# Kernel optimization log

Hardware: AMD Instinct MI355X
Metric: run time of the kernel (lower is better)

Reference implementation:

```python
import jax, jax.numpy as jnp
import numpy as np

B, S, D, U, L, DEG = 32, 256, 256, 256, 16, 16
N = B * S
E = N * DEG


def _xavier(k, shape, fan_in, fan_out):
    return jax.random.normal(k, shape, jnp.float32) * np.float32(np.sqrt(2.0 / (fan_in + fan_out)))


def setup_inputs() -> dict:
    key = jax.random.key(0)
    ks = jax.random.split(key, 16)
    src = jax.random.normal(ks[0], (S, B, D), jnp.float32)
    V_in = _xavier(ks[1], (L, D, U), D, U)
    b_in = jnp.zeros((L, U), jnp.float32)
    V_in_gate = _xavier(ks[2], (D, 1), D, 1)
    b_in_gate = jnp.ones((L, 1), jnp.float32)
    V_out = _xavier(ks[3], (L, D, U), D, U)
    b_out = jnp.zeros((L, U), jnp.float32)
    V_out_gate = _xavier(ks[4], (D, 1), D, 1)
    b_out_gate = jnp.ones((L, 1), jnp.float32)
    W_self_loop = _xavier(ks[5], (D, U), D, U)
    W_self_loop_gate = _xavier(ks[6], (D, 1), D, 1)
    arc_tensor_in = jnp.stack([jax.random.randint(ks[7], (E,), 0, B),
                               jax.random.randint(ks[8], (E,), 0, S)]).astype(jnp.int64)
    arc_tensor_out = jnp.stack([jax.random.randint(ks[9], (E,), 0, B),
                                jax.random.randint(ks[10], (E,), 0, S)]).astype(jnp.int64)
    label_tensor_in = jax.random.randint(ks[11], (1, E), 0, L).astype(jnp.int64)
    label_tensor_out = jax.random.randint(ks[12], (1, E), 0, L).astype(jnp.int64)
    mask_in = jnp.ones((N, DEG), jnp.float32)
    mask_out = jnp.ones((N, DEG), jnp.float32)
    mask_loop = jnp.ones((N, 1), jnp.float32)
    sent_mask = jnp.ones((S, B), jnp.float32)
    return {"src": src, "V_in": V_in, "b_in": b_in, "V_in_gate": V_in_gate,
            "b_in_gate": b_in_gate, "V_out": V_out, "b_out": b_out,
            "V_out_gate": V_out_gate, "b_out_gate": b_out_gate,
            "W_self_loop": W_self_loop, "W_self_loop_gate": W_self_loop_gate,
            "arc_tensor_in": arc_tensor_in, "arc_tensor_out": arc_tensor_out,
            "label_tensor_in": label_tensor_in, "label_tensor_out": label_tensor_out,
            "mask_in": mask_in, "mask_out": mask_out, "mask_loop": mask_loop,
            "sent_mask": sent_mask}


def _gcn_forward(src, V_in, b_in, V_in_gate, b_in_gate, V_out, b_out, V_out_gate,
                 b_out_gate, W_self_loop, W_self_loop_gate, mask_in, mask_out,
                 mask_loop, sent_mask, arc_tensor_in, arc_tensor_out,
                 label_tensor_in, label_tensor_out):
    S_, B_, D_ = src.shape
    U_ = V_in.shape[-1]
    enc = jnp.transpose(src, (1, 0, 2))            # [B,S,D]
    x = enc.reshape(B_ * S_, D_)                   # [N,D]

    def arc_branch(V, b, Vg, bg, arc, lab):
        # per-label transform of all nodes, as in the original: [L,N,U]
        all_lab = jnp.einsum('nd,ldu->lnu', x, V)
        idx = arc[0] * S_ + arc[1]                 # [E] flat node indices
        l = lab[0]                                  # [E] edge labels
        feats = all_lab[l, idx] + b[l]              # [E,U]
        deg = idx.shape[0] // (B_ * S_)
        feats = feats.reshape(B_, S_, deg, U_)
        g = (x @ Vg)[idx, 0] + bg[l, 0]             # [E]
        gate = g.reshape(B_, S_, deg)
        return feats, gate

    in_, in_gate = arc_branch(V_in, b_in, V_in_gate, b_in_gate, arc_tensor_in, label_tensor_in)
    out_, out_gate = arc_branch(V_out, b_out, V_out_gate, b_out_gate, arc_tensor_out, label_tensor_out)
    same = (x @ W_self_loop).reshape(B_, S_, 1, U_)
    same_gate = (x @ W_self_loop_gate).reshape(B_, S_, 1)

    pot = jnp.concatenate([in_, out_, same], axis=2)            # [B,S,maxdeg,U]
    pot_gate = jnp.concatenate([in_gate, out_gate, same_gate], axis=2)
    mask_soft = jnp.concatenate([mask_in, mask_out, mask_loop], axis=1)  # [N,maxdeg]
    md = pot.shape[2]
    pot = pot.reshape(B_ * S_, md, U_)
    probs = jax.nn.sigmoid(pot_gate.reshape(B_ * S_, md)) * mask_soft
    res = jax.nn.relu(jnp.sum(pot * probs[:, :, None], axis=1)).reshape(B_, S_, U_)
    res = res * sent_mask.T[:, :, None]
    return jnp.transpose(res, (1, 0, 2))            # [S,B,U]


def reference(src, V_in, b_in, V_in_gate, b_in_gate, V_out, b_out, V_out_gate,
              b_out_gate, W_self_loop, W_self_loop_gate, arc_tensor_in,
              arc_tensor_out, label_tensor_in, label_tensor_out, mask_in,
              mask_out, mask_loop, sent_mask):
    return _gcn_forward(src, V_in, b_in, V_in_gate, b_in_gate, V_out, b_out,
                        V_out_gate, b_out_gate, W_self_loop, W_self_loop_gate,
                        mask_in, mask_out, mask_loop, sent_mask,
                        arc_tensor_in, arc_tensor_out, label_tensor_in,
                        label_tensor_out)
```

## Files before the change

### kernel.cpp

```cpp
#include <hip/hip_runtime.h>
#include <hip/hip_bf16.h>

#define BB 32
#define SS 256
#define DD 256
#define UU 256
#define LL 16
#define DEG 16
#define NN (BB * SS)
#define EE (NN * DEG)
#define NSLICE 33
#define KMAIN (NSLICE * DD)
#define KEXT 256
#define KTOT (KMAIN + KEXT)
#define KSPLIT 8
#define KS (KTOT / KSPLIT)
#define TM 128
#define TN 256

using short8 = __attribute__((ext_vector_type(8))) short;
using f32x4  = __attribute__((ext_vector_type(4))) float;

#define GLDS(g, l)                                                        \
  __builtin_amdgcn_global_load_lds(                                       \
      (const __attribute__((address_space(1))) void*)(g),                 \
      (__attribute__((address_space(3))) void*)(l), 16, 0, 0)

__device__ __forceinline__ float bf2f(unsigned short v) {
  union { unsigned u; float f; } t;
  t.u = ((unsigned)v) << 16;
  return t.f;
}
__device__ __forceinline__ unsigned short f2bf(float f) {
  __hip_bfloat16 h = __float2bfloat16(f);
  return *(unsigned short*)&h;
}
__device__ __forceinline__ float sigm(float x) {
  return 1.f / (1.f + __expf(-x));
}

__global__ __launch_bounds__(256) void k_pre(
    const float* __restrict__ src, const float* __restrict__ gin,
    const float* __restrict__ gout, const float* __restrict__ gloop,
    const float* __restrict__ Vin, const float* __restrict__ Vout,
    const float* __restrict__ Wself, const float* __restrict__ b_in,
    const float* __restrict__ b_out,
    __hip_bfloat16* __restrict__ x_bf, float* __restrict__ xg_in,
    float* __restrict__ xg_out, float* __restrict__ xg_loop,
    __hip_bfloat16* __restrict__ Vt) {
  int bid = blockIdx.x;
  if (bid < NN) {
    int n = bid;
    int b = n / SS, s = n % SS;
    int d = threadIdx.x;
    float v = src[(size_t)(s * BB + b) * DD + d];
    x_bf[(size_t)n * DD + d] = __float2bfloat16(v);
    float p0 = v * gin[d], p1 = v * gout[d], p2 = v * gloop[d];
#pragma unroll
    for (int o = 32; o > 0; o >>= 1) {
      p0 += __shfl_down(p0, o);
      p1 += __shfl_down(p1, o);
      p2 += __shfl_down(p2, o);
    }
    __shared__ float r0[4], r1[4], r2[4];
    int w = threadIdx.x >> 6, lane = threadIdx.x & 63;
    if (lane == 0) { r0[w] = p0; r1[w] = p1; r2[w] = p2; }
    __syncthreads();
    if (threadIdx.x == 0) {
      xg_in[n]   = r0[0] + r0[1] + r0[2] + r0[3];
      xg_out[n]  = r1[0] + r1[1] + r1[2] + r1[3];
      xg_loop[n] = r2[0] + r2[1] + r2[2] + r2[3];
    }
    return;
  }
  int t = bid - NN;
  int z = t >> 6;
  int rem = t & 63;
  int bx = rem & 7, by = rem >> 3;
  int tid = threadIdx.x;
  int tx = tid & 31, ty = tid >> 5;
  if (z == NSLICE) {
    int u0 = bx * 32, j0 = by * 32;
#pragma unroll
    for (int i = 0; i < 4; i++) {
      int u = u0 + ty + i * 8, j = j0 + tx;
      float v = 0.f;
      if (j >= 1 && j <= LL)         v = b_in[(j - 1) * UU + u];
      else if (j > LL && j < NSLICE) v = b_out[(j - 1 - LL) * UU + u];
      Vt[(size_t)u * KTOT + KMAIN + j] = __float2bfloat16(v);
    }
    return;
  }
  __shared__ float tbuf[32][33];
  const float* srcM = (z == 0) ? Wself
                    : (z <= LL ? Vin  + (size_t)(z - 1)      * DD * UU
                               : Vout + (size_t)(z - 1 - LL) * DD * UU);
  int u0 = bx * 32, d0 = by * 32;
#pragma unroll
  for (int i = 0; i < 4; i++) {
    int dr = ty + i * 8;
    tbuf[dr][tx] = srcM[(size_t)(d0 + dr) * UU + u0 + tx];
  }
  __syncthreads();
#pragma unroll
  for (int i = 0; i < 4; i++) {
    int ur = ty + i * 8;
    Vt[(size_t)(u0 + ur) * KTOT + z * DD + d0 + tx] = __float2bfloat16(tbuf[tx][ur]);
  }
}

__global__ __launch_bounds__(64) void k_agg(
    const __hip_bfloat16* __restrict__ x,
    const float* __restrict__ xg_in, const float* __restrict__ xg_out,
    const float* __restrict__ xg_loop,
    const float* __restrict__ b_ing, const float* __restrict__ b_outg,
    const int* __restrict__ arc_in, const int* __restrict__ arc_out,
    const int* __restrict__ lab_in, const int* __restrict__ lab_out,
    const float* __restrict__ mask_in, const float* __restrict__ mask_out,
    const float* __restrict__ mask_loop,
    __hip_bfloat16* __restrict__ Y) {
  __shared__ int u_sl[32], u_src[32];
  __shared__ float u_w[32];
  __shared__ int s_sl[32], s_src[32];
  __shared__ float s_w[32];
  __shared__ float s_wsum[NSLICE];
  int n = blockIdx.x, tid = threadIdx.x;
  if (tid < 32) {
    int br = tid >> 4, k = tid & 15;
    int e = n * DEG + k;
    const int* a = br ? arc_out : arc_in;
    int l = (br ? lab_out : lab_in)[e];
    int srcn = a[e] * SS + a[EE + e];
    float g = (br ? xg_out : xg_in)[srcn] + (br ? b_outg : b_ing)[l];
    u_sl[tid] = 1 + br * LL + l;
    u_src[tid] = srcn;
    u_w[tid] = sigm(g) * (br ? mask_out : mask_in)[e];
  }
  __syncthreads();
  if (tid < 32) {
    int my = u_sl[tid];
    int rank = 0;
#pragma unroll
    for (int j = 0; j < 32; j++) {
      int oj = u_sl[j];
      rank += (oj < my || (oj == my && j < tid)) ? 1 : 0;
    }
    s_sl[rank] = my;
    s_src[rank] = u_src[tid];
    s_w[rank] = u_w[tid];
  }
  __syncthreads();

  const unsigned short* xp = (const unsigned short*)x;
  unsigned short* yp = (unsigned short*)Y;
  size_t base = (size_t)n * KTOT;
  int d4 = tid * 4;
  {
    float wl = sigm(xg_loop[n]) * mask_loop[n];
    ushort4 v = *(const ushort4*)&xp[(size_t)n * DD + d4];
    ushort4 o;
    o.x = f2bf(wl * bf2f(v.x)); o.y = f2bf(wl * bf2f(v.y));
    o.z = f2bf(wl * bf2f(v.z)); o.w = f2bf(wl * bf2f(v.w));
    *(ushort4*)&yp[base + d4] = o;
  }
  unsigned long long present = 0ull;
  float a0 = 0.f, a1 = 0.f, a2 = 0.f, a3 = 0.f, ws = 0.f;
#pragma unroll
  for (int e = 0; e < 32; e++) {
    int sl = s_sl[e];
    int srcn = s_src[e];
    float w = s_w[e];
    ushort4 v = *(const ushort4*)&xp[(size_t)srcn * DD + d4];
    a0 += w * bf2f(v.x); a1 += w * bf2f(v.y);
    a2 += w * bf2f(v.z); a3 += w * bf2f(v.w);
    ws += w;
    int slnext = (e < 31) ? s_sl[e + 1] : 999;
    if (sl != slnext) {
      ushort4 o;
      o.x = f2bf(a0); o.y = f2bf(a1); o.z = f2bf(a2); o.w = f2bf(a3);
      *(ushort4*)&yp[base + sl * DD + d4] = o;
      if (tid == 0) s_wsum[sl] = ws;
      present |= (1ull << sl);
      a0 = a1 = a2 = a3 = ws = 0.f;
    }
  }
  ushort4 zero4 = {0, 0, 0, 0};
#pragma unroll
  for (int s = 1; s < NSLICE; s++) {
    if (!((present >> s) & 1ull)) {
      *(ushort4*)&yp[base + s * DD + d4] = zero4;
      if (tid == 0) s_wsum[s] = 0.f;
    }
  }
  __syncthreads();
  {
    ushort4 o;
    unsigned short* op = (unsigned short*)&o;
#pragma unroll
    for (int c = 0; c < 4; c++) {
      int j = d4 + c;
      float v = (j >= 1 && j < NSLICE) ? s_wsum[j] : 0.f;
      op[c] = f2bf(v);
    }
    *(ushort4*)&yp[base + KMAIN + d4] = o;
  }
}

__global__ __launch_bounds__(256, 2) void k_gemm(
    const __hip_bfloat16* __restrict__ A, const __hip_bfloat16* __restrict__ Bt,
    __hip_bfloat16* __restrict__ partial) {
  __shared__ __align__(16) __hip_bfloat16 As[2][TM * 32];
  __shared__ __align__(16) __hip_bfloat16 Bs[2][TN * 32];
  __hip_bfloat16* P = partial + (size_t)blockIdx.y * NN * UU;
  int kbeg = blockIdx.y * KS;
  int row0 = blockIdx.x * TM;
  int tid = threadIdx.x;
  int w = tid >> 6, lane = tid & 63;
  int lrow = lane & 15, quad = lane >> 4;
  int sr = lane >> 2;
  int sc = (lane & 3) * 8;

#define STAGE(bufi, k0)                                                     \
  {                                                                         \
    _Pragma("unroll")                                                       \
    for (int t = 0; t < 2; t++) {                                           \
      int rb = (w * 2 + t) * 16;                                            \
      GLDS(&A[(size_t)(row0 + rb + sr) * KTOT + (k0) + sc],                 \
           &As[bufi][rb * 32]);                                             \
    }                                                                       \
    _Pragma("unroll")                                                       \
    for (int t = 0; t < 4; t++) {                                           \
      int rb = (w * 4 + t) * 16;                                            \
      GLDS(&Bt[(size_t)(rb + sr) * KTOT + (k0) + sc], &Bs[bufi][rb * 32]);  \
    }                                                                       \
  }

  STAGE(0, kbeg);
  f32x4 acc[8][4] = {};
  constexpr int NIT = KS / 32;
  for (int it = 0; it < NIT; it++) {
    int cur = it & 1;
    __syncthreads();
    if (it + 1 < NIT) STAGE(cur ^ 1, kbeg + (it + 1) * 32);
    short8 af[8], bfr[4];
#pragma unroll
    for (int i = 0; i < 8; i++)
      af[i] = *(const short8*)&As[cur][(i * 16 + lrow) * 32 + quad * 8];
#pragma unroll
    for (int j = 0; j < 4; j++)
      bfr[j] = *(const short8*)&Bs[cur][(w * 64 + j * 16 + lrow) * 32 + quad * 8];
#pragma unroll
    for (int j = 0; j < 4; j++)
#pragma unroll
      for (int i = 0; i < 8; i++)
        acc[i][j] = __builtin_amdgcn_mfma_f32_16x16x32_bf16(af[i], bfr[j], acc[i][j], 0, 0, 0);
  }
#undef STAGE
#pragma unroll
  for (int i = 0; i < 8; i++)
#pragma unroll
    for (int j = 0; j < 4; j++) {
      int col = w * 64 + j * 16 + lrow;
      int rowb = row0 + i * 16 + quad * 4;
#pragma unroll
      for (int r = 0; r < 4; r++)
        P[(size_t)(rowb + r) * UU + col] = __float2bfloat16(acc[i][j][r]);
    }
}

__global__ __launch_bounds__(64) void k_finish(
    const __hip_bfloat16* __restrict__ partial, const float* __restrict__ sent,
    float* __restrict__ out) {
  int n = blockIdx.x, u4 = threadIdx.x * 4;
  size_t idx = (size_t)n * UU + u4;
  const unsigned short* pp = (const unsigned short*)partial;
  float a0 = 0.f, a1 = 0.f, a2 = 0.f, a3 = 0.f;
#pragma unroll
  for (int z = 0; z < KSPLIT; z++) {
    ushort4 v = *(const ushort4*)&pp[(size_t)z * NN * UU + idx];
    a0 += bf2f(v.x); a1 += bf2f(v.y); a2 += bf2f(v.z); a3 += bf2f(v.w);
  }
  int s = n % SS, b = n / SS;
  float sm = sent[s * BB + b];
  float4 o;
  o.x = fmaxf(a0, 0.f) * sm; o.y = fmaxf(a1, 0.f) * sm;
  o.z = fmaxf(a2, 0.f) * sm; o.w = fmaxf(a3, 0.f) * sm;
  *(float4*)&out[((size_t)s * BB + b) * UU + u4] = o;
}

extern "C" void kernel_launch(void* const* d_in, const int* in_sizes, int n_in,
                              void* d_out, int out_size, void* d_ws, size_t ws_size,
                              hipStream_t stream) {
  const float* src      = (const float*)d_in[0];
  const float* V_in     = (const float*)d_in[1];
  const float* b_in     = (const float*)d_in[2];
  const float* V_ing    = (const float*)d_in[3];
  const float* b_ing    = (const float*)d_in[4];
  const float* V_out    = (const float*)d_in[5];
  const float* b_out    = (const float*)d_in[6];
  const float* V_outg   = (const float*)d_in[7];
  const float* b_outg   = (const float*)d_in[8];
  const float* W_self   = (const float*)d_in[9];
  const float* W_selfg  = (const float*)d_in[10];
  const int* arc_in     = (const int*)d_in[11];
  const int* arc_out    = (const int*)d_in[12];
  const int* lab_in     = (const int*)d_in[13];
  const int* lab_out    = (const int*)d_in[14];
  const float* mask_in  = (const float*)d_in[15];
  const float* mask_out = (const float*)d_in[16];
  const float* mask_loop= (const float*)d_in[17];
  const float* sent     = (const float*)d_in[18];
  float* out = (float*)d_out;

  char* ws = (char*)d_ws;
  size_t off = 0;
  auto alloc = [&](size_t bytes) -> void* {
    void* p = ws + off;
    off += (bytes + 255) & ~(size_t)255;
    return p;
  };
  __hip_bfloat16* x_bf = (__hip_bfloat16*)alloc((size_t)NN * DD * 2);
  __hip_bfloat16* Vt   = (__hip_bfloat16*)alloc((size_t)UU * KTOT * 2);
  float* xg_in   = (float*)alloc(NN * 4);
  float* xg_out  = (float*)alloc(NN * 4);
  float* xg_loop = (float*)alloc(NN * 4);
  __hip_bfloat16* Y = (__hip_bfloat16*)alloc((size_t)NN * KTOT * 2);
  __hip_bfloat16* partial =
      (__hip_bfloat16*)alloc((size_t)KSPLIT * NN * UU * 2);

  k_pre<<<NN + (NSLICE + 1) * 64, 256, 0, stream>>>(
      src, V_ing, V_outg, W_selfg, V_in, V_out, W_self, b_in, b_out,
      x_bf, xg_in, xg_out, xg_loop, Vt);
  k_agg<<<NN, 64, 0, stream>>>(x_bf, xg_in, xg_out, xg_loop, b_ing, b_outg,
                               arc_in, arc_out, lab_in, lab_out,
                               mask_in, mask_out, mask_loop, Y);
  k_gemm<<<dim3(NN / TM, KSPLIT), 256, 0, stream>>>(Y, Vt, partial);
  k_finish<<<NN, 64, 0, stream>>>(partial, sent, out);
}
```

Measured before the change: 192.4 us.

## Fuse neighbor aggregation into GEMM A-tile construction, drop materialized Y

Instead of materializing the large aggregated matrix Y (N x ~8.7K bf16) in a separate kernel, a small metadata kernel writes sorted edge lists, per-slice offsets and weight sums. The GEMM then builds each A tile on the fly by gathering source rows of x and weighting them, with K split into 17 chunks of two slices each and the M tile reduced to 64 rows. This removes the write and re-read of Y, but adds irregular gathers inside the GEMM main loop and a larger partial buffer for k_finish to reduce.

```diff
diff --git a/kernel.cpp b/kernel.cpp
--- a/kernel.cpp
+++ b/kernel.cpp
@@ -13,9 +13,8 @@
 #define KMAIN (NSLICE * DD)
 #define KEXT 256
 #define KTOT (KMAIN + KEXT)
-#define KSPLIT 8
-#define KS (KTOT / KSPLIT)
-#define TM 128
+#define KSPLIT 17
+#define TM 64
 #define TN 256
 
 using short8 = __attribute__((ext_vector_type(8))) short;
@@ -109,8 +108,7 @@
   }
 }
 
-__global__ __launch_bounds__(64) void k_agg(
-    const __hip_bfloat16* __restrict__ x,
+__global__ __launch_bounds__(64) void k_meta(
     const float* __restrict__ xg_in, const float* __restrict__ xg_out,
     const float* __restrict__ xg_loop,
     const float* __restrict__ b_ing, const float* __restrict__ b_outg,
@@ -118,12 +116,10 @@
     const int* __restrict__ lab_in, const int* __restrict__ lab_out,
     const float* __restrict__ mask_in, const float* __restrict__ mask_out,
     const float* __restrict__ mask_loop,
-    __hip_bfloat16* __restrict__ Y) {
+    int2* __restrict__ ed, unsigned char* __restrict__ off,
+    float* __restrict__ wsumbuf) {
   __shared__ int u_sl[32], u_src[32];
   __shared__ float u_w[32];
-  __shared__ int s_sl[32], s_src[32];
-  __shared__ float s_w[32];
-  __shared__ float s_wsum[NSLICE];
   int n = blockIdx.x, tid = threadIdx.x;
   if (tid < 32) {
     int br = tid >> 4, k = tid & 15;
@@ -145,106 +141,97 @@
       int oj = u_sl[j];
       rank += (oj < my || (oj == my && j < tid)) ? 1 : 0;
     }
-    s_sl[rank] = my;
-    s_src[rank] = u_src[tid];
-    s_w[rank] = u_w[tid];
-  }
-  __syncthreads();
-
-  const unsigned short* xp = (const unsigned short*)x;
-  unsigned short* yp = (unsigned short*)Y;
-  size_t base = (size_t)n * KTOT;
-  int d4 = tid * 4;
-  {
+    ed[(size_t)n * 34 + 1 + rank] =
+        make_int2(u_src[tid] | (my << 16), __float_as_int(u_w[tid]));
+  }
+  if (tid == 32) {
     float wl = sigm(xg_loop[n]) * mask_loop[n];
-    ushort4 v = *(const ushort4*)&xp[(size_t)n * DD + d4];
-    ushort4 o;
-    o.x = f2bf(wl * bf2f(v.x)); o.y = f2bf(wl * bf2f(v.y));
-    o.z = f2bf(wl * bf2f(v.z)); o.w = f2bf(wl * bf2f(v.w));
-    *(ushort4*)&yp[base + d4] = o;
-  }
-  unsigned long long present = 0ull;
-  float a0 = 0.f, a1 = 0.f, a2 = 0.f, a3 = 0.f, ws = 0.f;
-#pragma unroll
-  for (int e = 0; e < 32; e++) {
-    int sl = s_sl[e];
-    int srcn = s_src[e];
-    float w = s_w[e];
-    ushort4 v = *(const ushort4*)&xp[(size_t)srcn * DD + d4];
-    a0 += w * bf2f(v.x); a1 += w * bf2f(v.y);
-    a2 += w * bf2f(v.z); a3 += w * bf2f(v.w);
-    ws += w;
-    int slnext = (e < 31) ? s_sl[e + 1] : 999;
-    if (sl != slnext) {
-      ushort4 o;
-      o.x = f2bf(a0); o.y = f2bf(a1); o.z = f2bf(a2); o.w = f2bf(a3);
-      *(ushort4*)&yp[base + sl * DD + d4] = o;
-      if (tid == 0) s_wsum[sl] = ws;
-      present |= (1ull << sl);
-      a0 = a1 = a2 = a3 = ws = 0.f;
-    }
-  }
-  ushort4 zero4 = {0, 0, 0, 0};
-#pragma unroll
-  for (int s = 1; s < NSLICE; s++) {
-    if (!((present >> s) & 1ull)) {
-      *(ushort4*)&yp[base + s * DD + d4] = zero4;
-      if (tid == 0) s_wsum[s] = 0.f;
-    }
-  }
-  __syncthreads();
-  {
-    ushort4 o;
-    unsigned short* op = (unsigned short*)&o;
-#pragma unroll
-    for (int c = 0; c < 4; c++) {
-      int j = d4 + c;
-      float v = (j >= 1 && j < NSLICE) ? s_wsum[j] : 0.f;
-      op[c] = f2bf(v);
-    }
-    *(ushort4*)&yp[base + KMAIN + d4] = o;
-  }
-}
-
-__global__ __launch_bounds__(256, 2) void k_gemm(
-    const __hip_bfloat16* __restrict__ A, const __hip_bfloat16* __restrict__ Bt,
-    __hip_bfloat16* __restrict__ partial) {
+    ed[(size_t)n * 34] = make_int2(n, __float_as_int(wl));
+  }
+  if (tid < 35) {
+    int cnt = 0;
+#pragma unroll
+    for (int j = 0; j < 32; j++) cnt += (u_sl[j] < tid) ? 1 : 0;
+    off[(size_t)n * 36 + tid] = (unsigned char)((tid >= 1 ? 1 : 0) + cnt);
+  }
+  float ws = 0.f;
+  if (tid >= 1 && tid < 33) {
+#pragma unroll
+    for (int j = 0; j < 32; j++) ws += (u_sl[j] == tid) ? u_w[j] : 0.f;
+  }
+  if (tid < 34) wsumbuf[(size_t)n * 34 + tid] = ws;
+}
+
+__global__ __launch_bounds__(256, 3) void k_gemm(
+    const __hip_bfloat16* __restrict__ x, const __hip_bfloat16* __restrict__ Bt,
+    const int2* __restrict__ ed, const unsigned char* __restrict__ off,
+    const float* __restrict__ wsumbuf, __hip_bfloat16* __restrict__ partial) {
   __shared__ __align__(16) __hip_bfloat16 As[2][TM * 32];
   __shared__ __align__(16) __hip_bfloat16 Bs[2][TN * 32];
-  __hip_bfloat16* P = partial + (size_t)blockIdx.y * NN * UU;
-  int kbeg = blockIdx.y * KS;
+  int z = blockIdx.y;
+  __hip_bfloat16* P = partial + (size_t)z * NN * UU;
   int row0 = blockIdx.x * TM;
   int tid = threadIdx.x;
   int w = tid >> 6, lane = tid & 63;
   int lrow = lane & 15, quad = lane >> 4;
-  int sr = lane >> 2;
-  int sc = (lane & 3) * 8;
-
-#define STAGE(bufi, k0)                                                     \
-  {                                                                         \
-    _Pragma("unroll")                                                       \
-    for (int t = 0; t < 2; t++) {                                           \
-      int rb = (w * 2 + t) * 16;                                            \
-      GLDS(&A[(size_t)(row0 + rb + sr) * KTOT + (k0) + sc],                 \
-           &As[bufi][rb * 32]);                                             \
-    }                                                                       \
-    _Pragma("unroll")                                                       \
-    for (int t = 0; t < 4; t++) {                                           \
-      int rb = (w * 4 + t) * 16;                                            \
-      GLDS(&Bt[(size_t)(rb + sr) * KTOT + (k0) + sc], &Bs[bufi][rb * 32]);  \
-    }                                                                       \
-  }
-
-  STAGE(0, kbeg);
-  f32x4 acc[8][4] = {};
-  constexpr int NIT = KS / 32;
+  int sr = lane >> 2, sc = (lane & 3) * 8;
+  int r = tid >> 2, q = tid & 3;
+  int n = row0 + r;
+  const unsigned short* xp = (const unsigned short*)x;
+
+  auto STAGEB = [&](int bufi, int it) {
+    int s = 2 * z + (it >> 3);
+    int k0 = s * 256 + (it & 7) * 32;
+#pragma unroll
+    for (int t = 0; t < 4; t++) {
+      int rb = (w * 4 + t) * 16;
+      GLDS(&Bt[(size_t)(rb + sr) * KTOT + k0 + sc], &Bs[bufi][rb * 32]);
+    }
+  };
+
+  auto BUILD = [&](int bufi, int it) {
+    int s = 2 * z + (it >> 3);
+    int dcol0 = (it & 7) * 32 + q * 8;
+    float a[8] = {0.f, 0.f, 0.f, 0.f, 0.f, 0.f, 0.f, 0.f};
+    if (s < 33) {
+      int lo = off[(size_t)n * 36 + s];
+      int hi = off[(size_t)n * 36 + s + 1];
+      for (int e = lo; e < hi; e++) {
+        int2 m = ed[(size_t)n * 34 + e];
+        int srcn = m.x & 0xFFFF;
+        float wv = __int_as_float(m.y);
+        short8 v = *(const short8*)&xp[(size_t)srcn * DD + dcol0];
+#pragma unroll
+        for (int i = 0; i < 8; i++)
+          a[i] += wv * bf2f((unsigned short)v[i]);
+      }
+    } else {
+#pragma unroll
+      for (int i = 0; i < 8; i++) {
+        int j = dcol0 + i;
+        a[i] = (j < 34) ? wsumbuf[(size_t)n * 34 + j] : 0.f;
+      }
+    }
+    short8 o;
+#pragma unroll
+    for (int i = 0; i < 8; i++) o[i] = (short)f2bf(a[i]);
+    *(short8*)&As[bufi][r * 32 + q * 8] = o;
+  };
+
+  STAGEB(0, 0);
+  BUILD(0, 0);
+  f32x4 acc[4][4] = {};
+  constexpr int NIT = 16;
   for (int it = 0; it < NIT; it++) {
     int cur = it & 1;
     __syncthreads();
-    if (it + 1 < NIT) STAGE(cur ^ 1, kbeg + (it + 1) * 32);
-    short8 af[8], bfr[4];
-#pragma unroll
-    for (int i = 0; i < 8; i++)
+    if (it + 1 < NIT) {
+      STAGEB(cur ^ 1, it + 1);
+      BUILD(cur ^ 1, it + 1);
+    }
+    short8 af[4], bfr[4];
+#pragma unroll
+    for (int i = 0; i < 4; i++)
       af[i] = *(const short8*)&As[cur][(i * 16 + lrow) * 32 + quad * 8];
 #pragma unroll
     for (int j = 0; j < 4; j++)
@@ -252,19 +239,18 @@
 #pragma unroll
     for (int j = 0; j < 4; j++)
 #pragma unroll
-      for (int i = 0; i < 8; i++)
+      for (int i = 0; i < 4; i++)
         acc[i][j] = __builtin_amdgcn_mfma_f32_16x16x32_bf16(af[i], bfr[j], acc[i][j], 0, 0, 0);
   }
-#undef STAGE
-#pragma unroll
-  for (int i = 0; i < 8; i++)
+#pragma unroll
+  for (int i = 0; i < 4; i++)
 #pragma unroll
     for (int j = 0; j < 4; j++) {
       int col = w * 64 + j * 16 + lrow;
       int rowb = row0 + i * 16 + quad * 4;
 #pragma unroll
-      for (int r = 0; r < 4; r++)
-        P[(size_t)(rowb + r) * UU + col] = __float2bfloat16(acc[i][j][r]);
+      for (int rr = 0; rr < 4; rr++)
+        P[(size_t)(rowb + rr) * UU + col] = __float2bfloat16(acc[i][j][rr]);
     }
 }
 
@@ -313,10 +299,10 @@
   float* out = (float*)d_out;
 
   char* ws = (char*)d_ws;
-  size_t off = 0;
+  size_t off_b = 0;
   auto alloc = [&](size_t bytes) -> void* {
-    void* p = ws + off;
-    off += (bytes + 255) & ~(size_t)255;
+    void* p = ws + off_b;
+    off_b += (bytes + 255) & ~(size_t)255;
     return p;
   };
   __hip_bfloat16* x_bf = (__hip_bfloat16*)alloc((size_t)NN * DD * 2);
@@ -324,16 +310,20 @@
   float* xg_in   = (float*)alloc(NN * 4);
   float* xg_out  = (float*)alloc(NN * 4);
   float* xg_loop = (float*)alloc(NN * 4);
-  __hip_bfloat16* Y = (__hip_bfloat16*)alloc((size_t)NN * KTOT * 2);
+  int2* ed       = (int2*)alloc((size_t)NN * 34 * 8);
+  unsigned char* offb = (unsigned char*)alloc((size_t)NN * 36);
+  float* wsumbuf = (float*)alloc((size_t)NN * 34 * 4);
   __hip_bfloat16* partial =
       (__hip_bfloat16*)alloc((size_t)KSPLIT * NN * UU * 2);
 
   k_pre<<<NN + (NSLICE + 1) * 64, 256, 0, stream>>>(
       src, V_ing, V_outg, W_selfg, V_in, V_out, W_self, b_in, b_out,
       x_bf, xg_in, xg_out, xg_loop, Vt);
-  k_agg<<<NN, 64, 0, stream>>>(x_bf, xg_in, xg_out, xg_loop, b_ing, b_outg,
-                               arc_in, arc_out, lab_in, lab_out,
-                               mask_in, mask_out, mask_loop, Y);
-  k_gemm<<<dim3(NN / TM, KSPLIT), 256, 0, stream>>>(Y, Vt, partial);
+  k_meta<<<NN, 64, 0, stream>>>(xg_in, xg_out, xg_loop, b_ing, b_outg,
+                                arc_in, arc_out, lab_in, lab_out,
+                                mask_in, mask_out, mask_loop,
+                                ed, offb, wsumbuf);
+  k_gemm<<<dim3(NN / TM, KSPLIT), 256, 0, stream>>>(x_bf, Vt, ed, offb,
+                                                    wsumbuf, partial);
   k_finish<<<NN, 64, 0, stream>>>(partial, sent, out);
 }
```

Result: slower. 238.0 us (+23.7%).

## Store aggregated Y slice-major, double the GEMM K-split, pack four nodes per block

Applied to the files above, without the earlier changes.

The aggregated activation matrix Y moves from node-major rows of length KTOT to a slice-major layout [slice][node][D]. Each GEMM K-tile now reads a contiguous D-row block from one slice. KSPLIT goes from 8 to 16 to put more blocks on the GPU. The aggregation and finish kernels now handle four nodes per 256-thread block instead of one per 64-thread block, which cuts block-launch overhead. The doubled split-K writes and reads twice as much partial-sum data, and the finish kernel has twice as many slices to add up.

```diff
diff --git a/kernel.cpp b/kernel.cpp
--- a/kernel.cpp
+++ b/kernel.cpp
@@ -10,10 +10,10 @@
 #define NN (BB * SS)
 #define EE (NN * DEG)
 #define NSLICE 33
+#define NSL2 34
 #define KMAIN (NSLICE * DD)
-#define KEXT 256
-#define KTOT (KMAIN + KEXT)
-#define KSPLIT 8
+#define KTOT (NSL2 * DD)
+#define KSPLIT 16
 #define KS (KTOT / KSPLIT)
 #define TM 128
 #define TN 256
@@ -109,7 +109,7 @@
   }
 }
 
-__global__ __launch_bounds__(64) void k_agg(
+__global__ __launch_bounds__(256) void k_agg(
     const __hip_bfloat16* __restrict__ x,
     const float* __restrict__ xg_in, const float* __restrict__ xg_out,
     const float* __restrict__ xg_loop,
@@ -119,67 +119,67 @@
     const float* __restrict__ mask_in, const float* __restrict__ mask_out,
     const float* __restrict__ mask_loop,
     __hip_bfloat16* __restrict__ Y) {
-  __shared__ int u_sl[32], u_src[32];
-  __shared__ float u_w[32];
-  __shared__ int s_sl[32], s_src[32];
-  __shared__ float s_w[32];
-  __shared__ float s_wsum[NSLICE];
-  int n = blockIdx.x, tid = threadIdx.x;
-  if (tid < 32) {
-    int br = tid >> 4, k = tid & 15;
+  __shared__ int u_sl[4][32], u_src[4][32];
+  __shared__ float u_w[4][32];
+  __shared__ int s_sl[4][32], s_src[4][32];
+  __shared__ float s_w[4][32];
+  __shared__ float s_wsum[4][NSLICE];
+  int wv = threadIdx.x >> 6, lane = threadIdx.x & 63;
+  int n = blockIdx.x * 4 + wv;
+  if (lane < 32) {
+    int br = lane >> 4, k = lane & 15;
     int e = n * DEG + k;
     const int* a = br ? arc_out : arc_in;
     int l = (br ? lab_out : lab_in)[e];
     int srcn = a[e] * SS + a[EE + e];
     float g = (br ? xg_out : xg_in)[srcn] + (br ? b_outg : b_ing)[l];
-    u_sl[tid] = 1 + br * LL + l;
-    u_src[tid] = srcn;
-    u_w[tid] = sigm(g) * (br ? mask_out : mask_in)[e];
+    u_sl[wv][lane] = 1 + br * LL + l;
+    u_src[wv][lane] = srcn;
+    u_w[wv][lane] = sigm(g) * (br ? mask_out : mask_in)[e];
   }
   __syncthreads();
-  if (tid < 32) {
-    int my = u_sl[tid];
+  if (lane < 32) {
+    int my = u_sl[wv][lane];
     int rank = 0;
 #pragma unroll
     for (int j = 0; j < 32; j++) {
-      int oj = u_sl[j];
-      rank += (oj < my || (oj == my && j < tid)) ? 1 : 0;
-    }
-    s_sl[rank] = my;
-    s_src[rank] = u_src[tid];
-    s_w[rank] = u_w[tid];
+      int oj = u_sl[wv][j];
+      rank += (oj < my || (oj == my && j < lane)) ? 1 : 0;
+    }
+    s_sl[wv][rank] = my;
+    s_src[wv][rank] = u_src[wv][lane];
+    s_w[wv][rank] = u_w[wv][lane];
   }
   __syncthreads();
 
   const unsigned short* xp = (const unsigned short*)x;
   unsigned short* yp = (unsigned short*)Y;
-  size_t base = (size_t)n * KTOT;
-  int d4 = tid * 4;
+  int d4 = lane * 4;
   {
     float wl = sigm(xg_loop[n]) * mask_loop[n];
     ushort4 v = *(const ushort4*)&xp[(size_t)n * DD + d4];
     ushort4 o;
     o.x = f2bf(wl * bf2f(v.x)); o.y = f2bf(wl * bf2f(v.y));
     o.z = f2bf(wl * bf2f(v.z)); o.w = f2bf(wl * bf2f(v.w));
-    *(ushort4*)&yp[base + d4] = o;
+    *(ushort4*)&yp[(size_t)n * DD + d4] = o;
   }
   unsigned long long present = 0ull;
   float a0 = 0.f, a1 = 0.f, a2 = 0.f, a3 = 0.f, ws = 0.f;
 #pragma unroll
   for (int e = 0; e < 32; e++) {
-    int sl = s_sl[e];
-    int srcn = s_src[e];
-    float w = s_w[e];
+    int sl = s_sl[wv][e];
+    int srcn = s_src[wv][e];
+    float w = s_w[wv][e];
     ushort4 v = *(const ushort4*)&xp[(size_t)srcn * DD + d4];
     a0 += w * bf2f(v.x); a1 += w * bf2f(v.y);
     a2 += w * bf2f(v.z); a3 += w * bf2f(v.w);
     ws += w;
-    int slnext = (e < 31) ? s_sl[e + 1] : 999;
+    int slnext = (e < 31) ? s_sl[wv][e + 1] : 999;
     if (sl != slnext) {
       ushort4 o;
       o.x = f2bf(a0); o.y = f2bf(a1); o.z = f2bf(a2); o.w = f2bf(a3);
-      *(ushort4*)&yp[base + sl * DD + d4] = o;
-      if (tid == 0) s_wsum[sl] = ws;
+      *(ushort4*)&yp[((size_t)sl * NN + n) * DD + d4] = o;
+      if (lane == 0) s_wsum[wv][sl] = ws;
       present |= (1ull << sl);
       a0 = a1 = a2 = a3 = ws = 0.f;
     }
@@ -188,8 +188,8 @@
 #pragma unroll
   for (int s = 1; s < NSLICE; s++) {
     if (!((present >> s) & 1ull)) {
-      *(ushort4*)&yp[base + s * DD + d4] = zero4;
-      if (tid == 0) s_wsum[s] = 0.f;
+      *(ushort4*)&yp[((size_t)s * NN + n) * DD + d4] = zero4;
+      if (lane == 0) s_wsum[wv][s] = 0.f;
     }
   }
   __syncthreads();
@@ -199,10 +199,10 @@
 #pragma unroll
     for (int c = 0; c < 4; c++) {
       int j = d4 + c;
-      float v = (j >= 1 && j < NSLICE) ? s_wsum[j] : 0.f;
+      float v = (j >= 1 && j < NSLICE) ? s_wsum[wv][j] : 0.f;
       op[c] = f2bf(v);
     }
-    *(ushort4*)&yp[base + KMAIN + d4] = o;
+    *(ushort4*)&yp[((size_t)NSLICE * NN + n) * DD + d4] = o;
   }
 }
 
@@ -220,28 +220,30 @@
   int sr = lane >> 2;
   int sc = (lane & 3) * 8;
 
-#define STAGE(bufi, k0)                                                     \
+#define STAGE(bufi, it)                                                     \
   {                                                                         \
+    int k0 = kbeg + (it) * 32;                                              \
+    int sl = k0 >> 8, dc = k0 & 255;                                        \
+    const __hip_bfloat16* Ab = A + ((size_t)sl * NN + row0) * DD + dc;      \
     _Pragma("unroll")                                                       \
     for (int t = 0; t < 2; t++) {                                           \
       int rb = (w * 2 + t) * 16;                                            \
-      GLDS(&A[(size_t)(row0 + rb + sr) * KTOT + (k0) + sc],                 \
-           &As[bufi][rb * 32]);                                             \
+      GLDS(&Ab[(size_t)(rb + sr) * DD + sc], &As[bufi][rb * 32]);           \
     }                                                                       \
     _Pragma("unroll")                                                       \
     for (int t = 0; t < 4; t++) {                                           \
       int rb = (w * 4 + t) * 16;                                            \
-      GLDS(&Bt[(size_t)(rb + sr) * KTOT + (k0) + sc], &Bs[bufi][rb * 32]);  \
+      GLDS(&Bt[(size_t)(rb + sr) * KTOT + k0 + sc], &Bs[bufi][rb * 32]);    \
     }                                                                       \
   }
 
-  STAGE(0, kbeg);
+  STAGE(0, 0);
   f32x4 acc[8][4] = {};
   constexpr int NIT = KS / 32;
   for (int it = 0; it < NIT; it++) {
     int cur = it & 1;
     __syncthreads();
-    if (it + 1 < NIT) STAGE(cur ^ 1, kbeg + (it + 1) * 32);
+    if (it + 1 < NIT) STAGE(cur ^ 1, it + 1);
     short8 af[8], bfr[4];
 #pragma unroll
     for (int i = 0; i < 8; i++)
@@ -268,10 +270,12 @@
     }
 }
 
-__global__ __launch_bounds__(64) void k_finish(
+__global__ __launch_bounds__(256) void k_finish(
     const __hip_bfloat16* __restrict__ partial, const float* __restrict__ sent,
     float* __restrict__ out) {
-  int n = blockIdx.x, u4 = threadIdx.x * 4;
+  int wv = threadIdx.x >> 6, lane = threadIdx.x & 63;
+  int n = blockIdx.x * 4 + wv;
+  int u4 = lane * 4;
   size_t idx = (size_t)n * UU + u4;
   const unsigned short* pp = (const unsigned short*)partial;
   float a0 = 0.f, a1 = 0.f, a2 = 0.f, a3 = 0.f;
@@ -324,16 +328,16 @@
   float* xg_in   = (float*)alloc(NN * 4);
   float* xg_out  = (float*)alloc(NN * 4);
   float* xg_loop = (float*)alloc(NN * 4);
-  __hip_bfloat16* Y = (__hip_bfloat16*)alloc((size_t)NN * KTOT * 2);
+  __hip_bfloat16* Y = (__hip_bfloat16*)alloc((size_t)NSL2 * NN * DD * 2);
   __hip_bfloat16* partial =
       (__hip_bfloat16*)alloc((size_t)KSPLIT * NN * UU * 2);
 
   k_pre<<<NN + (NSLICE + 1) * 64, 256, 0, stream>>>(
       src, V_ing, V_outg, W_selfg, V_in, V_out, W_self, b_in, b_out,
       x_bf, xg_in, xg_out, xg_loop, Vt);
-  k_agg<<<NN, 64, 0, stream>>>(x_bf, xg_in, xg_out, xg_loop, b_ing, b_outg,
-                               arc_in, arc_out, lab_in, lab_out,
-                               mask_in, mask_out, mask_loop, Y);
+  k_agg<<<NN / 4, 256, 0, stream>>>(x_bf, xg_in, xg_out, xg_loop, b_ing, b_outg,
+                                    arc_in, arc_out, lab_in, lab_out,
+                                    mask_in, mask_out, mask_loop, Y);
   k_gemm<<<dim3(NN / TM, KSPLIT), 256, 0, stream>>>(Y, Vt, partial);
-  k_finish<<<NN, 64, 0, stream>>>(partial, sent, out);
-}
+  k_finish<<<NN / 4, 256, 0, stream>>>(partial, sent, out);
+}
```

Result: slower. 204.8 us (+6.4%).
